# Kernel tuning notes

Hardware: AMD Instinct MI355X
Metric: run time of the kernel (lower is better)

Reference implementation:

```python
import math
import jax, jax.numpy as jnp
import numpy as np

D_MODEL = 1024
D_INNER = 2048   # expand=2
D_STATE = 16
D_CONV = 4
DT_RANK = 64     # ceil(d_model/16)
N_LAYER = 8
INPUT_DIM = 256
BATCH = 16
TT = 64
S_IN = 13
EPS = 1e-5


def setup_inputs() -> dict:
    key = jax.random.key(0)
    ks = jax.random.split(key, 10)
    def nrm(k, shape, s):
        return jax.random.normal(k, shape, dtype=jnp.float32) * jnp.float32(s)
    a_row = jnp.log(jnp.arange(1, D_STATE + 1, dtype=jnp.float32))
    return {
        "x": jax.random.normal(ks[0], (BATCH * TT, S_IN, INPUT_DIM), dtype=jnp.float32),
        "tt": TT,
        "w_in": nrm(ks[1], (D_MODEL, INPUT_DIM), 1.0 / np.sqrt(INPUT_DIM)),
        "b_in": jnp.zeros((D_MODEL,), jnp.float32),
        "cls": nrm(ks[2], (1, 1, D_MODEL), 1.0),
        "norm_w": jnp.ones((N_LAYER, D_MODEL), jnp.float32),
        "in_proj_w": nrm(ks[3], (N_LAYER, 2 * D_INNER, D_MODEL), 1.0 / np.sqrt(D_MODEL)),
        "conv_w": nrm(ks[4], (N_LAYER, D_INNER, D_CONV), 0.3),
        "conv_b": jnp.zeros((N_LAYER, D_INNER), jnp.float32),
        "x_proj_w": nrm(ks[5], (N_LAYER, DT_RANK + 2 * D_STATE, D_INNER), 1.0 / np.sqrt(D_INNER)),
        "dt_proj_w": nrm(ks[6], (N_LAYER, D_INNER, DT_RANK), 1.0 / np.sqrt(DT_RANK)),
        "dt_proj_b": jnp.float32(-4.0) + nrm(ks[7], (N_LAYER, D_INNER), 0.1),
        "A_log": jnp.tile(a_row, (N_LAYER, D_INNER, 1)),
        "D_param": jnp.ones((N_LAYER, D_INNER), jnp.float32),
        "out_proj_w": nrm(ks[8], (N_LAYER, D_MODEL, D_INNER), 1.0 / np.sqrt(D_INNER)),
        "normf_w": jnp.ones((D_MODEL,), jnp.float32),
    }


def _rmsnorm(u, w):
    return u * jax.lax.rsqrt(jnp.mean(u * u, axis=-1, keepdims=True) + EPS) * w


def _mamba_mixer(u, ipw, cw, cb, xpw, dtw, dtb, Alog, Dp, opw):
    # u: (b, L, d_model)
    b, L, _ = u.shape
    xz = u @ ipw.T                              # (b, L, 2*di)
    di = xz.shape[-1] // 2
    xm, z = xz[..., :di], xz[..., di:]
    # causal depthwise conv1d, kernel D_CONV, truncated to L (torch padding=K-1 then [:L])
    K = cw.shape[-1]
    xp = jnp.pad(xm, ((0, 0), (K - 1, 0), (0, 0)))
    xc = cb
    for k in range(K):
        xc = xc + cw[:, k] * xp[:, k:k + L, :]
    xc = jax.nn.silu(xc)                        # (b, L, di)
    proj = xc @ xpw.T                           # (b, L, dt_rank + 2*ds)
    ds = Alog.shape[-1]
    dtr = proj.shape[-1] - 2 * ds
    dt = jax.nn.softplus(proj[..., :dtr] @ dtw.T + dtb)   # (b, L, di)
    Bm = proj[..., dtr:dtr + ds]                # (b, L, ds)
    Cm = proj[..., dtr + ds:]                   # (b, L, ds)
    A = -jnp.exp(Alog)                          # (di, ds)

    def step(hst, ins):
        dt_t, B_t, C_t, u_t = ins               # (b,di),(b,ds),(b,ds),(b,di)
        dA = jnp.exp(dt_t[..., None] * A)                       # (b, di, ds)
        dBu = dt_t[..., None] * B_t[:, None, :] * u_t[..., None]
        hst = dA * hst + dBu
        y_t = jnp.einsum('bds,bs->bd', hst, C_t)
        return hst, y_t

    h0 = jnp.zeros((b, di, ds), u.dtype)
    _, ys = jax.lax.scan(step, h0, (dt.transpose(1, 0, 2), Bm.transpose(1, 0, 2),
                                    Cm.transpose(1, 0, 2), xc.transpose(1, 0, 2)))
    y = ys.transpose(1, 0, 2) + Dp * xc
    y = y * jax.nn.silu(z)
    return y @ opw.T                            # (b, L, d_model)


def _forward(x, tt, w_in, b_in, cls, norm_w, in_proj_w, conv_w, conv_b,
             x_proj_w, dt_proj_w, dt_proj_b, A_log, D_param, out_proj_w, normf_w):
    BF, Sin, _ = x.shape
    b = BF // tt
    d = w_in.shape[0]
    h = x @ w_in.T + b_in                       # (BF, Sin, d)
    h = h.reshape(b, tt, Sin, d)
    # use_aux_tokens=False -> reward+reset and action tokens are zeros
    cls_tok = jnp.broadcast_to(cls, (b, tt, 1, d))
    z_tok = jnp.zeros((b, tt, 1, d), h.dtype)
    tokens = jnp.concatenate([cls_tok, h, z_tok, z_tok], axis=2)   # (b, tt, S, d)
    S = Sin + 3
    # sinusoidal positional encoding over tt steps, shared across S tokens of a step
    pos = jnp.arange(tt, dtype=jnp.float32)
    div = jnp.exp(jnp.arange(0, d, 2, dtype=jnp.float32) * jnp.float32(-math.log(10000.0) / d))
    ang = pos[:, None] * div[None, :]
    pe = jnp.stack([jnp.sin(ang), jnp.cos(ang)], axis=-1).reshape(tt, d)
    seq = (tokens + pe[None, :, None, :]).reshape(b, tt * S, d)

    def layer_fn(carry, p):
        hs, res = carry
        nw, ipw, cw, cb, xpw, dtw, dtb, Alog, Dp, opw = p
        res = hs + res                           # residual add (res starts at 0 == None branch)
        hn = _rmsnorm(res, nw)
        hs = _mamba_mixer(hn, ipw, cw, cb, xpw, dtw, dtb, Alog, Dp, opw)
        return (hs, res), None

    params = (norm_w, in_proj_w, conv_w, conv_b, x_proj_w,
              dt_proj_w, dt_proj_b, A_log, D_param, out_proj_w)
    (hs, res), _ = jax.lax.scan(layer_fn, (seq, jnp.zeros_like(seq)), params)
    hidden = _rmsnorm(hs + res, normf_w)         # dropout p=0 is identity
    hidden = hidden.reshape(b, tt, S, d)
    pooled = hidden[:, :, 0, :]                  # pool='cls', tt != 1
    return pooled.reshape(b * tt, d)


def reference(x, tt, w_in, b_in, cls, norm_w, in_proj_w, conv_w, conv_b,
              x_proj_w, dt_proj_w, dt_proj_b, A_log, D_param, out_proj_w, normf_w):
    return _forward(x, tt, w_in, b_in, cls, norm_w, in_proj_w, conv_w, conv_b,
                    x_proj_w, dt_proj_w, dt_proj_b, A_log, D_param, out_proj_w, normf_w)
```

## Files before the change

### kernel.cpp

```cpp
#include <hip/hip_runtime.h>
#include <hip/hip_bf16.h>
#include <math.h>

#define D_MODEL 1024
#define D_INNER 2048
#define D_STATE 16
#define D_CONV 4
#define DT_RANK 64
#define N_LAYER 8
#define INPUT_DIM 256
#define BATCH 16
#define TT 64
#define S_IN 13
#define SEQ_S 16
#define L_SEQ 1024
#define XZ_LD (2 * D_INNER)
#define PROJ_N 96
#define EPS 1e-5f

typedef __attribute__((ext_vector_type(8))) short short8;
typedef __attribute__((ext_vector_type(4))) float f32x4;

__device__ __forceinline__ unsigned short f2bu(float x) {
  unsigned int u = __float_as_uint(x);
  unsigned int r = (u + 0x7fffu + ((u >> 16) & 1u)) >> 16;
  return (unsigned short)r;
}

__device__ __forceinline__ void gload_lds16(const void* g, void* l) {
  __builtin_amdgcn_global_load_lds(
      (const __attribute__((address_space(1))) void*)g,
      (__attribute__((address_space(3))) void*)l, 16, 0, 0);
}

__global__ __launch_bounds__(256) void gemm_mfma(
    const unsigned short* __restrict__ A, int lda,
    const unsigned short* __restrict__ W, int ldw,
    const float* __restrict__ bias,
    float* __restrict__ C, int ldc, size_t cPartStride,
    unsigned short* __restrict__ Cb, int ldcb,
    int M, int N, int kLen, int act)
{
  __shared__ unsigned short As[128 * 32];
  __shared__ unsigned short Ws[128 * 32];
  const int tid  = threadIdx.x;
  const int wave = tid >> 6;
  const int lane = tid & 63;
  const int m0 = blockIdx.x * 128;
  const int n0 = blockIdx.y * 128;
  const int wm = (wave & 1) * 64;
  const int wn = (wave >> 1) * 64;
  const int kStart = blockIdx.z * kLen;
  C += (size_t)blockIdx.z * cPartStride;

  const int srow = (lane >> 2);
  const int scol = (lane & 3) * 8;

  f32x4 acc[4][4] = {};

  for (int k0 = kStart; k0 < kStart + kLen; k0 += 32) {
#pragma unroll
    for (int i = 0; i < 2; ++i) {
      int rowA = m0 + wave * 32 + i * 16 + srow;
      if (rowA > M - 1) rowA = M - 1;
      gload_lds16(A + (size_t)rowA * lda + k0 + scol,
                  &As[(wave * 32 + i * 16) * 32]);
      int rowW = n0 + wave * 32 + i * 16 + srow;
      if (rowW > N - 1) rowW = N - 1;
      gload_lds16(W + (size_t)rowW * ldw + k0 + scol,
                  &Ws[(wave * 32 + i * 16) * 32]);
    }
    __syncthreads();

    short8 af[4], bf[4];
#pragma unroll
    for (int mi = 0; mi < 4; ++mi)
      af[mi] = *(const short8*)&As[(wm + mi * 16 + (lane & 15)) * 32 + (lane >> 4) * 8];
#pragma unroll
    for (int ni = 0; ni < 4; ++ni)
      bf[ni] = *(const short8*)&Ws[(wn + ni * 16 + (lane & 15)) * 32 + (lane >> 4) * 8];
#pragma unroll
    for (int mi = 0; mi < 4; ++mi)
#pragma unroll
      for (int ni = 0; ni < 4; ++ni)
        acc[mi][ni] = __builtin_amdgcn_mfma_f32_16x16x32_bf16(
            af[mi], bf[ni], acc[mi][ni], 0, 0, 0);
    __syncthreads();
  }

#pragma unroll
  for (int mi = 0; mi < 4; ++mi) {
#pragma unroll
    for (int ni = 0; ni < 4; ++ni) {
      const int col = n0 + wn + ni * 16 + (lane & 15);
      if (col >= N) continue;
#pragma unroll
      for (int r = 0; r < 4; ++r) {
        const int row = m0 + wm + mi * 16 + (lane >> 4) * 4 + r;
        if (row >= M) continue;
        float v = acc[mi][ni][r];
        if (bias) v += bias[col];
        if (act == 1) v = (v > 20.f) ? v : log1pf(__expf(v));
        C[(size_t)row * ldc + col] = v;
        if (Cb) Cb[(size_t)row * ldcb + col] = f2bu(v);
      }
    }
  }
}

__global__ __launch_bounds__(256) void xproj_combine(
    const float* __restrict__ part, float* __restrict__ proj,
    unsigned short* __restrict__ projb, int n4, size_t stride4)
{
  int i = blockIdx.x * 256 + threadIdx.x;
  if (i >= n4) return;
  float4 a = ((const float4*)part)[i];
  float4 b = ((const float4*)part)[i + stride4];
  float4 c = ((const float4*)part)[i + 2 * stride4];
  float4 d = ((const float4*)part)[i + 3 * stride4];
  float4 v = make_float4(a.x + b.x + c.x + d.x, a.y + b.y + c.y + d.y,
                         a.z + b.z + c.z + d.z, a.w + b.w + c.w + d.w);
  ((float4*)proj)[i] = v;
  ushort4 o;
  o.x = f2bu(v.x); o.y = f2bu(v.y); o.z = f2bu(v.z); o.w = f2bu(v.w);
  ((ushort4*)projb)[i] = o;
}

__global__ __launch_bounds__(256) void cvt_bf16(
    const float* __restrict__ in, unsigned short* __restrict__ out, int n4)
{
  int i = blockIdx.x * 256 + threadIdx.x;
  if (i < n4) {
    float4 v = ((const float4*)in)[i];
    ushort4 o;
    o.x = f2bu(v.x); o.y = f2bu(v.y); o.z = f2bu(v.z); o.w = f2bu(v.w);
    ((ushort4*)out)[i] = o;
  }
}

__device__ __forceinline__ float block_reduce_sum_256(float v)
{
  __shared__ float red[4];
#pragma unroll
  for (int off = 32; off > 0; off >>= 1) v += __shfl_xor(v, off, 64);
  const int tid = threadIdx.x;
  if ((tid & 63) == 0) red[tid >> 6] = v;
  __syncthreads();
  return red[0] + red[1] + red[2] + red[3];
}

__global__ __launch_bounds__(256) void seq_build(
    const float* __restrict__ hflat, const float* __restrict__ cls,
    float* __restrict__ hs, float* __restrict__ res)
{
  const int row = blockIdx.x;
  const int bl = row >> 10;
  const int l = row & (L_SEQ - 1);
  const int t = l >> 4;
  const int s = l & 15;
  const int tid = threadIdx.x;

  float4 v;
  if (s == 0) {
    v = ((const float4*)cls)[tid];
  } else if (s <= S_IN) {
    const size_t hrow = ((size_t)(bl * TT + t) * S_IN + (s - 1)) * D_MODEL;
    v = ((const float4*)(hflat + hrow))[tid];
  } else {
    v = make_float4(0.f, 0.f, 0.f, 0.f);
  }

  const float cexp = -logf(10000.f) / (float)D_MODEL;
  float pe[4];
#pragma unroll
  for (int j = 0; j < 4; ++j) {
    int d = tid * 4 + j;
    int i2 = d & ~1;
    float ang = (float)t * expf((float)i2 * cexp);
    pe[j] = (d & 1) ? cosf(ang) : sinf(ang);
  }
  v.x += pe[0]; v.y += pe[1]; v.z += pe[2]; v.w += pe[3];

  const size_t base = (size_t)row * D_MODEL;
  ((float4*)(hs + base))[tid] = v;
  ((float4*)(res + base))[tid] = make_float4(0.f, 0.f, 0.f, 0.f);
}

__global__ __launch_bounds__(256) void add_rmsnorm(
    float* __restrict__ res, const float* __restrict__ hs,
    unsigned short* __restrict__ hnb, const float* __restrict__ w)
{
  const int row = blockIdx.x;
  const int tid = threadIdx.x;
  const size_t base = (size_t)row * D_MODEL;
  float4 r = ((const float4*)(res + base))[tid];
  float4 h = ((const float4*)(hs + base))[tid];
  r.x += h.x; r.y += h.y; r.z += h.z; r.w += h.w;
  ((float4*)(res + base))[tid] = r;
  float ss = r.x * r.x + r.y * r.y + r.z * r.z + r.w * r.w;
  ss = block_reduce_sum_256(ss);
  const float scale = rsqrtf(ss * (1.f / (float)D_MODEL) + EPS);
  float4 wv = ((const float4*)w)[tid];
  ushort4 o;
  o.x = f2bu(r.x * scale * wv.x);
  o.y = f2bu(r.y * scale * wv.y);
  o.z = f2bu(r.z * scale * wv.z);
  o.w = f2bu(r.w * scale * wv.w);
  ((ushort4*)(hnb + base))[tid] = o;
}

__global__ __launch_bounds__(256) void conv_silu(
    const float* __restrict__ xz, const float* __restrict__ cw,
    const float* __restrict__ cb, float* __restrict__ xc,
    unsigned short* __restrict__ xcb)
{
  const int c = blockIdx.x * 256 + threadIdx.x;
  const int t = blockIdx.y;
  const int bl = blockIdx.z;
  const size_t row = (size_t)bl * L_SEQ + t;

  const float w0 = cw[c * D_CONV + 0];
  const float w1 = cw[c * D_CONV + 1];
  const float w2 = cw[c * D_CONV + 2];
  const float w3 = cw[c * D_CONV + 3];

  float acc = cb[c];
  if (t >= 3) acc = fmaf(w0, xz[(row - 3) * XZ_LD + c], acc);
  if (t >= 2) acc = fmaf(w1, xz[(row - 2) * XZ_LD + c], acc);
  if (t >= 1) acc = fmaf(w2, xz[(row - 1) * XZ_LD + c], acc);
  acc = fmaf(w3, xz[row * XZ_LD + c], acc);

  acc = acc / (1.f + __expf(-acc));
  xc[row * D_INNER + c] = acc;
  xcb[row * D_INNER + c] = f2bu(acc);
}

__global__ __launch_bounds__(256) void scan4(
    const float* __restrict__ xz, const float* __restrict__ xc,
    const float* __restrict__ proj,
    const float* __restrict__ Alog, const float* __restrict__ Dp,
    unsigned short* __restrict__ yb)
{
  const int tid  = threadIdx.x;
  const int lane = tid & 63;
  const int wave = tid >> 6;
  const int chl  = lane >> 2;
  const int sq   = lane & 3;
  const int ch   = blockIdx.x * 64 + wave * 16 + chl;
  const int s0   = sq * 4;
  const int bl   = blockIdx.y;
  const size_t base = (size_t)bl * L_SEQ;

  float A[4], h[4] = {0.f, 0.f, 0.f, 0.f};
#pragma unroll
  for (int k = 0; k < 4; ++k)
    A[k] = -__expf(Alog[(size_t)ch * D_STATE + s0 + k]);
  const float Dv = Dp[ch];

  float pdt[4], pz[4], pu[4];
  float4 pB[4], pC[4];

#define SCAN_LOAD(slot, t)                                                    \
  {                                                                           \
    const size_t r_ = base + (size_t)(t);                                     \
    pdt[slot] = xz[r_ * XZ_LD + ch];                                          \
    pz[slot]  = xz[r_ * XZ_LD + D_INNER + ch];                                \
    pu[slot]  = xc[r_ * D_INNER + ch];                                        \
    pB[slot]  = *(const float4*)&proj[r_ * PROJ_N + DT_RANK + s0];            \
    pC[slot]  = *(const float4*)&proj[r_ * PROJ_N + DT_RANK + D_STATE + s0];  \
  }

  SCAN_LOAD(0, 0)
  SCAN_LOAD(1, 1)
  SCAN_LOAD(2, 2)

#pragma unroll 4
  for (int t = 0; t < L_SEQ; ++t) {
    const int sl = t & 3;
    int tn = t + 3;
    if (tn > L_SEQ - 1) tn = L_SEQ - 1;
    SCAN_LOAD((t + 3) & 3, tn)

    const float dtv = pdt[sl];
    const float u   = pu[sl];
    const float du  = dtv * u;
    const float4 B4 = pB[sl];
    const float4 C4 = pC[sl];
    const float Bk[4] = {B4.x, B4.y, B4.z, B4.w};
    const float Ck[4] = {C4.x, C4.y, C4.z, C4.w};
    float yv = 0.f;
#pragma unroll
    for (int k = 0; k < 4; ++k) {
      const float dA = __expf(dtv * A[k]);
      h[k] = fmaf(dA, h[k], du * Bk[k]);
      yv = fmaf(h[k], Ck[k], yv);
    }
    yv += __shfl_xor(yv, 1, 64);
    yv += __shfl_xor(yv, 2, 64);
    if (sq == 0) {
      const float zv = pz[sl];
      const float g = zv / (1.f + __expf(-zv));
      yb[(base + t) * D_INNER + ch] = f2bu(fmaf(Dv, u, yv) * g);
    }
  }
#undef SCAN_LOAD
}

__global__ __launch_bounds__(256) void pool_norm(
    const float* __restrict__ hs, const float* __restrict__ res,
    const float* __restrict__ w, float* __restrict__ out, int b0)
{
  const int idx = blockIdx.x;
  const int bl = idx >> 6;
  const int t = idx & 63;
  const size_t base = ((size_t)bl * L_SEQ + (size_t)t * SEQ_S) * D_MODEL;
  const int tid = threadIdx.x;
  float4 h = ((const float4*)(hs + base))[tid];
  float4 r = ((const float4*)(res + base))[tid];
  float4 v = make_float4(h.x + r.x, h.y + r.y, h.z + r.z, h.w + r.w);
  float ss = v.x * v.x + v.y * v.y + v.z * v.z + v.w * v.w;
  ss = block_reduce_sum_256(ss);
  const float scale = rsqrtf(ss * (1.f / (float)D_MODEL) + EPS);
  float4 wv = ((const float4*)w)[tid];
  float4 o = make_float4(v.x * scale * wv.x, v.y * scale * wv.y,
                         v.z * scale * wv.z, v.w * scale * wv.w);
  const size_t orow = (size_t)((b0 + bl) * TT + t) * D_MODEL;
  ((float4*)(out + orow))[tid] = o;
}

extern "C" void kernel_launch(void* const* d_in, const int* in_sizes, int n_in,
                              void* d_out, int out_size, void* d_ws, size_t ws_size,
                              hipStream_t stream)
{
  const float* x      = (const float*)d_in[0];
  const float* w_in   = (const float*)d_in[2];
  const float* b_in   = (const float*)d_in[3];
  const float* cls    = (const float*)d_in[4];
  const float* norm_w = (const float*)d_in[5];
  const float* ipw    = (const float*)d_in[6];
  const float* cw     = (const float*)d_in[7];
  const float* cb     = (const float*)d_in[8];
  const float* xpw    = (const float*)d_in[9];
  const float* dtw    = (const float*)d_in[10];
  const float* dtb    = (const float*)d_in[11];
  const float* Alog   = (const float*)d_in[12];
  const float* Dp     = (const float*)d_in[13];
  const float* opw    = (const float*)d_in[14];
  const float* normfw = (const float*)d_in[15];
  float* out = (float*)d_out;

  const size_t N_WIN = (size_t)D_MODEL * INPUT_DIM;
  const size_t N_IPW = (size_t)N_LAYER * XZ_LD * D_MODEL;
  const size_t N_XPW = (size_t)N_LAYER * PROJ_N * D_INNER;
  const size_t N_DTW = (size_t)N_LAYER * D_INNER * DT_RANK;
  const size_t N_OPW = (size_t)N_LAYER * D_MODEL * D_INNER;
  const size_t N_XB  = (size_t)BATCH * TT * S_IN * INPUT_DIM;
  const size_t N_BF  = N_WIN + N_IPW + N_XPW + N_DTW + N_OPW + N_XB;

  const size_t perB = (size_t)L_SEQ * (8288 * 4 + 3168 * 2);
  int bc = 0;
  for (int c = 16; c >= 1; c >>= 1)
    if (N_BF * 2 + perB * (size_t)c <= ws_size) { bc = c; break; }
  if (bc == 0) return;

  const int R = bc * L_SEQ;

  unsigned short* w_in_b = (unsigned short*)d_ws;
  unsigned short* ipw_b  = w_in_b + N_WIN;
  unsigned short* xpw_b  = ipw_b + N_IPW;
  unsigned short* dtw_b  = xpw_b + N_XPW;
  unsigned short* opw_b  = dtw_b + N_DTW;
  unsigned short* x_b    = opw_b + N_OPW;
  float* res  = (float*)(x_b + N_XB);
  float* hs   = res + (size_t)R * D_MODEL;
  float* xz   = hs + (size_t)R * D_MODEL;
  float* xc   = xz + (size_t)R * XZ_LD;
  float* proj = xc + (size_t)R * D_INNER;
  unsigned short* hnb   = (unsigned short*)(proj + (size_t)R * PROJ_N);
  unsigned short* xcb   = hnb + (size_t)R * D_MODEL;
  unsigned short* projb = xcb + (size_t)R * D_INNER;
  float* ppart = hs;

  cvt_bf16<<<(int)((N_WIN/4 + 255)/256), 256, 0, stream>>>(w_in, w_in_b, (int)(N_WIN/4));
  cvt_bf16<<<(int)((N_IPW/4 + 255)/256), 256, 0, stream>>>(ipw, ipw_b, (int)(N_IPW/4));
  cvt_bf16<<<(int)((N_XPW/4 + 255)/256), 256, 0, stream>>>(xpw, xpw_b, (int)(N_XPW/4));
  cvt_bf16<<<(int)((N_DTW/4 + 255)/256), 256, 0, stream>>>(dtw, dtw_b, (int)(N_DTW/4));
  cvt_bf16<<<(int)((N_OPW/4 + 255)/256), 256, 0, stream>>>(opw, opw_b, (int)(N_OPW/4));
  cvt_bf16<<<(int)((N_XB/4  + 255)/256), 256, 0, stream>>>(x,   x_b,   (int)(N_XB/4));

  for (int b0 = 0; b0 < BATCH; b0 += bc) {
    const int Mx = bc * TT * S_IN;
    float* hflat = xz;
    gemm_mfma<<<dim3((Mx + 127) / 128, D_MODEL / 128), 256, 0, stream>>>(
        x_b + (size_t)b0 * TT * S_IN * INPUT_DIM, INPUT_DIM,
        w_in_b, INPUT_DIM, b_in, hflat, D_MODEL, 0, nullptr, 0,
        Mx, D_MODEL, INPUT_DIM, 0);

    seq_build<<<R, 256, 0, stream>>>(hflat, cls, hs, res);

    for (int l = 0; l < N_LAYER; ++l) {
      add_rmsnorm<<<R, 256, 0, stream>>>(res, hs, hnb,
          norm_w + (size_t)l * D_MODEL);

      gemm_mfma<<<dim3(R / 128, XZ_LD / 128), 256, 0, stream>>>(
          hnb, D_MODEL, ipw_b + (size_t)l * XZ_LD * D_MODEL, D_MODEL,
          nullptr, xz, XZ_LD, 0, nullptr, 0, R, XZ_LD, D_MODEL, 0);

      conv_silu<<<dim3(D_INNER / 256, L_SEQ, bc), 256, 0, stream>>>(
          xz, cw + (size_t)l * D_INNER * D_CONV, cb + (size_t)l * D_INNER,
          xc, xcb);

      gemm_mfma<<<dim3(R / 128, 1, 4), 256, 0, stream>>>(
          xcb, D_INNER, xpw_b + (size_t)l * PROJ_N * D_INNER, D_INNER,
          nullptr, ppart, PROJ_N, (size_t)R * PROJ_N, nullptr, 0,
          R, PROJ_N, 512, 0);
      xproj_combine<<<(R * PROJ_N / 4 + 255) / 256, 256, 0, stream>>>(
          ppart, proj, projb, R * PROJ_N / 4, (size_t)R * PROJ_N / 4);

      gemm_mfma<<<dim3(R / 128, D_INNER / 128), 256, 0, stream>>>(
          projb, PROJ_N, dtw_b + (size_t)l * D_INNER * DT_RANK, DT_RANK,
          dtb + (size_t)l * D_INNER, xz, XZ_LD, 0, nullptr, 0,
          R, D_INNER, 64, 1);

      scan4<<<dim3(D_INNER / 64, bc), 256, 0, stream>>>(
          xz, xc, proj, Alog + (size_t)l * D_INNER * D_STATE,
          Dp + (size_t)l * D_INNER, xcb);

      gemm_mfma<<<dim3(R / 128, D_MODEL / 128), 256, 0, stream>>>(
          xcb, D_INNER, opw_b + (size_t)l * D_MODEL * D_INNER, D_INNER,
          nullptr, hs, D_MODEL, 0, nullptr, 0, R, D_MODEL, D_INNER, 0);
    }

    pool_norm<<<bc * TT, 256, 0, stream>>>(hs, res, normfw, out, b0);
  }
}
```

Measured before the change: 9.966 ms.

## Store intermediates in bf16 and fuse residual add into out_proj epilogue

```diff
diff --git a/kernel.cpp b/kernel.cpp
--- a/kernel.cpp
+++ b/kernel.cpp
@@ -26,6 +26,9 @@
   unsigned int r = (u + 0x7fffu + ((u >> 16) & 1u)) >> 16;
   return (unsigned short)r;
 }
+__device__ __forceinline__ float bu2f(unsigned short u) {
+  return __uint_as_float((unsigned int)u << 16);
+}
 
 __device__ __forceinline__ void gload_lds16(const void* g, void* l) {
   __builtin_amdgcn_global_load_lds(
@@ -37,7 +40,7 @@
     const unsigned short* __restrict__ A, int lda,
     const unsigned short* __restrict__ W, int ldw,
     const float* __restrict__ bias,
-    float* __restrict__ C, int ldc, size_t cPartStride,
+    float* __restrict__ C, int ldc, size_t cPartStride, int accum,
     unsigned short* __restrict__ Cb, int ldcb,
     int M, int N, int kLen, int act)
 {
@@ -51,7 +54,7 @@
   const int wm = (wave & 1) * 64;
   const int wn = (wave >> 1) * 64;
   const int kStart = blockIdx.z * kLen;
-  C += (size_t)blockIdx.z * cPartStride;
+  if (C) C += (size_t)blockIdx.z * cPartStride;
 
   const int srow = (lane >> 2);
   const int scol = (lane & 3) * 8;
@@ -101,7 +104,11 @@
         float v = acc[mi][ni][r];
         if (bias) v += bias[col];
         if (act == 1) v = (v > 20.f) ? v : log1pf(__expf(v));
-        C[(size_t)row * ldc + col] = v;
+        if (C) {
+          float o = v;
+          if (accum) o += C[(size_t)row * ldc + col];
+          C[(size_t)row * ldc + col] = o;
+        }
         if (Cb) Cb[(size_t)row * ldcb + col] = f2bu(v);
       }
     }
@@ -151,7 +158,7 @@
 
 __global__ __launch_bounds__(256) void seq_build(
     const float* __restrict__ hflat, const float* __restrict__ cls,
-    float* __restrict__ hs, float* __restrict__ res)
+    float* __restrict__ res)
 {
   const int row = blockIdx.x;
   const int bl = row >> 10;
@@ -181,22 +188,17 @@
   }
   v.x += pe[0]; v.y += pe[1]; v.z += pe[2]; v.w += pe[3];
 
-  const size_t base = (size_t)row * D_MODEL;
-  ((float4*)(hs + base))[tid] = v;
-  ((float4*)(res + base))[tid] = make_float4(0.f, 0.f, 0.f, 0.f);
-}
-
-__global__ __launch_bounds__(256) void add_rmsnorm(
-    float* __restrict__ res, const float* __restrict__ hs,
-    unsigned short* __restrict__ hnb, const float* __restrict__ w)
+  ((float4*)(res + (size_t)row * D_MODEL))[tid] = v;
+}
+
+__global__ __launch_bounds__(256) void rmsnorm_only(
+    const float* __restrict__ res, unsigned short* __restrict__ hnb,
+    const float* __restrict__ w)
 {
   const int row = blockIdx.x;
   const int tid = threadIdx.x;
   const size_t base = (size_t)row * D_MODEL;
   float4 r = ((const float4*)(res + base))[tid];
-  float4 h = ((const float4*)(hs + base))[tid];
-  r.x += h.x; r.y += h.y; r.z += h.z; r.w += h.w;
-  ((float4*)(res + base))[tid] = r;
   float ss = r.x * r.x + r.y * r.y + r.z * r.z + r.w * r.w;
   ss = block_reduce_sum_256(ss);
   const float scale = rsqrtf(ss * (1.f / (float)D_MODEL) + EPS);
@@ -210,9 +212,8 @@
 }
 
 __global__ __launch_bounds__(256) void conv_silu(
-    const float* __restrict__ xz, const float* __restrict__ cw,
-    const float* __restrict__ cb, float* __restrict__ xc,
-    unsigned short* __restrict__ xcb)
+    const unsigned short* __restrict__ xzb, const float* __restrict__ cw,
+    const float* __restrict__ cb, unsigned short* __restrict__ xcb)
 {
   const int c = blockIdx.x * 256 + threadIdx.x;
   const int t = blockIdx.y;
@@ -225,21 +226,19 @@
   const float w3 = cw[c * D_CONV + 3];
 
   float acc = cb[c];
-  if (t >= 3) acc = fmaf(w0, xz[(row - 3) * XZ_LD + c], acc);
-  if (t >= 2) acc = fmaf(w1, xz[(row - 2) * XZ_LD + c], acc);
-  if (t >= 1) acc = fmaf(w2, xz[(row - 1) * XZ_LD + c], acc);
-  acc = fmaf(w3, xz[row * XZ_LD + c], acc);
+  if (t >= 3) acc = fmaf(w0, bu2f(xzb[(row - 3) * XZ_LD + c]), acc);
+  if (t >= 2) acc = fmaf(w1, bu2f(xzb[(row - 2) * XZ_LD + c]), acc);
+  if (t >= 1) acc = fmaf(w2, bu2f(xzb[(row - 1) * XZ_LD + c]), acc);
+  acc = fmaf(w3, bu2f(xzb[row * XZ_LD + c]), acc);
 
   acc = acc / (1.f + __expf(-acc));
-  xc[row * D_INNER + c] = acc;
   xcb[row * D_INNER + c] = f2bu(acc);
 }
 
-__global__ __launch_bounds__(256) void scan4(
-    const float* __restrict__ xz, const float* __restrict__ xc,
+__global__ __launch_bounds__(256) void scan5(
+    const unsigned short* __restrict__ xzb, unsigned short* xcb,
     const float* __restrict__ proj,
-    const float* __restrict__ Alog, const float* __restrict__ Dp,
-    unsigned short* __restrict__ yb)
+    const float* __restrict__ Alog, const float* __restrict__ Dp)
 {
   const int tid  = threadIdx.x;
   const int lane = tid & 63;
@@ -263,9 +262,9 @@
 #define SCAN_LOAD(slot, t)                                                    \
   {                                                                           \
     const size_t r_ = base + (size_t)(t);                                     \
-    pdt[slot] = xz[r_ * XZ_LD + ch];                                          \
-    pz[slot]  = xz[r_ * XZ_LD + D_INNER + ch];                                \
-    pu[slot]  = xc[r_ * D_INNER + ch];                                        \
+    pdt[slot] = bu2f(xzb[r_ * XZ_LD + ch]);                                   \
+    pz[slot]  = bu2f(xzb[r_ * XZ_LD + D_INNER + ch]);                         \
+    pu[slot]  = bu2f(xcb[r_ * D_INNER + ch]);                                 \
     pB[slot]  = *(const float4*)&proj[r_ * PROJ_N + DT_RANK + s0];            \
     pC[slot]  = *(const float4*)&proj[r_ * PROJ_N + DT_RANK + D_STATE + s0];  \
   }
@@ -300,24 +299,22 @@
     if (sq == 0) {
       const float zv = pz[sl];
       const float g = zv / (1.f + __expf(-zv));
-      yb[(base + t) * D_INNER + ch] = f2bu(fmaf(Dv, u, yv) * g);
+      xcb[(base + t) * D_INNER + ch] = f2bu(fmaf(Dv, u, yv) * g);
     }
   }
 #undef SCAN_LOAD
 }
 
 __global__ __launch_bounds__(256) void pool_norm(
-    const float* __restrict__ hs, const float* __restrict__ res,
-    const float* __restrict__ w, float* __restrict__ out, int b0)
+    const float* __restrict__ res, const float* __restrict__ w,
+    float* __restrict__ out, int b0)
 {
   const int idx = blockIdx.x;
   const int bl = idx >> 6;
   const int t = idx & 63;
   const size_t base = ((size_t)bl * L_SEQ + (size_t)t * SEQ_S) * D_MODEL;
   const int tid = threadIdx.x;
-  float4 h = ((const float4*)(hs + base))[tid];
-  float4 r = ((const float4*)(res + base))[tid];
-  float4 v = make_float4(h.x + r.x, h.y + r.y, h.z + r.z, h.w + r.w);
+  float4 v = ((const float4*)(res + base))[tid];
   float ss = v.x * v.x + v.y * v.y + v.z * v.z + v.w * v.w;
   ss = block_reduce_sum_256(ss);
   const float scale = rsqrtf(ss * (1.f / (float)D_MODEL) + EPS);
@@ -357,7 +354,7 @@
   const size_t N_XB  = (size_t)BATCH * TT * S_IN * INPUT_DIM;
   const size_t N_BF  = N_WIN + N_IPW + N_XPW + N_DTW + N_OPW + N_XB;
 
-  const size_t perB = (size_t)L_SEQ * (8288 * 4 + 3168 * 2);
+  const size_t perB = (size_t)L_SEQ * 19008;
   int bc = 0;
   for (int c = 16; c >= 1; c >>= 1)
     if (N_BF * 2 + perB * (size_t)c <= ws_size) { bc = c; break; }
@@ -371,15 +368,14 @@
   unsigned short* dtw_b  = xpw_b + N_XPW;
   unsigned short* opw_b  = dtw_b + N_DTW;
   unsigned short* x_b    = opw_b + N_OPW;
-  float* res  = (float*)(x_b + N_XB);
-  float* hs   = res + (size_t)R * D_MODEL;
-  float* xz   = hs + (size_t)R * D_MODEL;
-  float* xc   = xz + (size_t)R * XZ_LD;
-  float* proj = xc + (size_t)R * D_INNER;
-  unsigned short* hnb   = (unsigned short*)(proj + (size_t)R * PROJ_N);
-  unsigned short* xcb   = hnb + (size_t)R * D_MODEL;
-  unsigned short* projb = xcb + (size_t)R * D_INNER;
-  float* ppart = hs;
+  float*          res  = (float*)(x_b + N_XB);
+  unsigned short* xzb  = (unsigned short*)(res + (size_t)R * D_MODEL);
+  unsigned short* xcb  = xzb + (size_t)R * XZ_LD;
+  float*          proj = (float*)(xcb + (size_t)R * D_INNER);
+  unsigned short* projb = (unsigned short*)(proj + (size_t)R * PROJ_N);
+  unsigned short* hnb   = projb + (size_t)R * PROJ_N;
+  float* ppart = (float*)hnb;
+  float* hflat = (float*)xzb;
 
   cvt_bf16<<<(int)((N_WIN/4 + 255)/256), 256, 0, stream>>>(w_in, w_in_b, (int)(N_WIN/4));
   cvt_bf16<<<(int)((N_IPW/4 + 255)/256), 256, 0, stream>>>(ipw, ipw_b, (int)(N_IPW/4));
@@ -390,47 +386,46 @@
 
   for (int b0 = 0; b0 < BATCH; b0 += bc) {
     const int Mx = bc * TT * S_IN;
-    float* hflat = xz;
     gemm_mfma<<<dim3((Mx + 127) / 128, D_MODEL / 128), 256, 0, stream>>>(
         x_b + (size_t)b0 * TT * S_IN * INPUT_DIM, INPUT_DIM,
-        w_in_b, INPUT_DIM, b_in, hflat, D_MODEL, 0, nullptr, 0,
+        w_in_b, INPUT_DIM, b_in, hflat, D_MODEL, 0, 0, nullptr, 0,
         Mx, D_MODEL, INPUT_DIM, 0);
 
-    seq_build<<<R, 256, 0, stream>>>(hflat, cls, hs, res);
+    seq_build<<<R, 256, 0, stream>>>(hflat, cls, res);
 
     for (int l = 0; l < N_LAYER; ++l) {
-      add_rmsnorm<<<R, 256, 0, stream>>>(res, hs, hnb,
+      rmsnorm_only<<<R, 256, 0, stream>>>(res, hnb,
           norm_w + (size_t)l * D_MODEL);
 
       gemm_mfma<<<dim3(R / 128, XZ_LD / 128), 256, 0, stream>>>(
           hnb, D_MODEL, ipw_b + (size_t)l * XZ_LD * D_MODEL, D_MODEL,
-          nullptr, xz, XZ_LD, 0, nullptr, 0, R, XZ_LD, D_MODEL, 0);
+          nullptr, nullptr, 0, 0, 0, xzb, XZ_LD, R, XZ_LD, D_MODEL, 0);
 
       conv_silu<<<dim3(D_INNER / 256, L_SEQ, bc), 256, 0, stream>>>(
-          xz, cw + (size_t)l * D_INNER * D_CONV, cb + (size_t)l * D_INNER,
-          xc, xcb);
+          xzb, cw + (size_t)l * D_INNER * D_CONV, cb + (size_t)l * D_INNER,
+          xcb);
 
       gemm_mfma<<<dim3(R / 128, 1, 4), 256, 0, stream>>>(
           xcb, D_INNER, xpw_b + (size_t)l * PROJ_N * D_INNER, D_INNER,
-          nullptr, ppart, PROJ_N, (size_t)R * PROJ_N, nullptr, 0,
+          nullptr, ppart, PROJ_N, (size_t)R * PROJ_N, 0, nullptr, 0,
           R, PROJ_N, 512, 0);
       xproj_combine<<<(R * PROJ_N / 4 + 255) / 256, 256, 0, stream>>>(
           ppart, proj, projb, R * PROJ_N / 4, (size_t)R * PROJ_N / 4);
 
       gemm_mfma<<<dim3(R / 128, D_INNER / 128), 256, 0, stream>>>(
           projb, PROJ_N, dtw_b + (size_t)l * D_INNER * DT_RANK, DT_RANK,
-          dtb + (size_t)l * D_INNER, xz, XZ_LD, 0, nullptr, 0,
+          dtb + (size_t)l * D_INNER, nullptr, 0, 0, 0, xzb, XZ_LD,
           R, D_INNER, 64, 1);
 
-      scan4<<<dim3(D_INNER / 64, bc), 256, 0, stream>>>(
-          xz, xc, proj, Alog + (size_t)l * D_INNER * D_STATE,
-          Dp + (size_t)l * D_INNER, xcb);
+      scan5<<<dim3(D_INNER / 64, bc), 256, 0, stream>>>(
+          xzb, xcb, proj, Alog + (size_t)l * D_INNER * D_STATE,
+          Dp + (size_t)l * D_INNER);
 
       gemm_mfma<<<dim3(R / 128, D_MODEL / 128), 256, 0, stream>>>(
           xcb, D_INNER, opw_b + (size_t)l * D_MODEL * D_INNER, D_INNER,
-          nullptr, hs, D_MODEL, 0, nullptr, 0, R, D_MODEL, D_INNER, 0);
+          nullptr, res, D_MODEL, 0, 1, nullptr, 0, R, D_MODEL, D_INNER, 0);
     }
 
-    pool_norm<<<bc * TT, 256, 0, stream>>>(hs, res, normfw, out, b0);
-  }
-}
+    pool_norm<<<bc * TT, 256, 0, stream>>>(res, normfw, out, b0);
+  }
+}
```

After: 8.443 ms. -15.3%, faster.
